# Kernel tuning notes

Hardware: AMD Instinct MI355X
Metric: run time of the kernel (lower is better)

## Reference

```python
import jax, jax.numpy as jnp
import numpy as np
from jax import lax

B, T, H, C = 64, 512, 1024, 8


def setup_inputs() -> dict:
    key = jax.random.key(0)
    ks = jax.random.split(key, 7)
    encoding = jax.random.normal(ks[0], (B, T, H), dtype=jnp.float32)
    labels = jax.random.randint(ks[1], (B, 3 * T), 0, C)
    W = jax.random.normal(ks[2], (3, C, H), dtype=jnp.float32) * 0.02
    b = jax.random.normal(ks[3], (3, C), dtype=jnp.float32) * 0.02
    start_trans = jax.random.normal(ks[4], (3, C), dtype=jnp.float32) * 0.1
    end_trans = jax.random.normal(ks[5], (3, C), dtype=jnp.float32) * 0.1
    trans = jax.random.normal(ks[6], (3, C, C), dtype=jnp.float32) * 0.1
    return {"encoding": encoding, "labels": labels, "W": W, "b": b,
            "start_trans": start_trans, "end_trans": end_trans, "trans": trans}


def crf_neg_log_lik(em, tags, start, end, trans):
    # em [B,T,C], tags [B,T] -> scalar (torchcrf reduction='sum', loss = -llh)
    bsz = em.shape[0]
    # numerator: score of gold path
    em_sc = jnp.take_along_axis(em, tags[:, :, None], axis=2)[..., 0].sum(axis=1)
    tr_sc = trans[tags[:, :-1], tags[:, 1:]].sum(axis=1)
    num = start[tags[:, 0]] + em_sc + tr_sc + end[tags[:, -1]]
    # denominator: forward algorithm (log partition)
    a0 = start[None, :] + em[:, 0]  # [B,C]

    def step(a, e_t):
        a_new = jax.nn.logsumexp(a[:, :, None] + trans[None] + e_t[:, None, :], axis=1)
        return a_new, None

    aT, _ = lax.scan(step, a0, jnp.moveaxis(em[:, 1:], 1, 0))
    logZ = jax.nn.logsumexp(aT + end[None, :], axis=1)
    return -(num - logZ).sum()


def viterbi(em, start, end, trans):
    # em [B,T,C] -> best tag path [B,T] (no mask: all sequences full length)
    v0 = start[None, :] + em[:, 0]

    def step(v, e_t):
        s = v[:, :, None] + trans[None]          # [B,C_prev,C_cur]
        bp = jnp.argmax(s, axis=1)               # [B,C]
        return jnp.max(s, axis=1) + e_t, bp

    vT, bps = lax.scan(step, v0, jnp.moveaxis(em[:, 1:], 1, 0))  # bps [T-1,B,C]
    last = jnp.argmax(vT + end[None, :], axis=1)  # [B]

    def back(tag, bp):
        prev = jnp.take_along_axis(bp, tag[:, None], axis=1)[:, 0]
        return prev, prev

    _, rev = lax.scan(back, last, bps, reverse=True)  # [T-1,B], tags for t=0..T-2
    tags = jnp.concatenate([rev, last[None]], axis=0)  # [T,B]
    return tags.T


def reference(encoding, labels, W, b, start_trans, end_trans, trans):
    # three per-task projections: logits [3,B,T,C]
    logits = jnp.einsum('bth,kch->kbtc', encoding, W) + b[:, None, None, :]
    tags = jnp.stack(jnp.split(labels, 3, axis=1))  # [3,B,T] (task/process/material)
    losses = jax.vmap(crf_neg_log_lik)(logits, tags, start_trans, end_trans, trans)
    loss = losses.sum()
    pred = jax.vmap(viterbi)(logits, start_trans, end_trans, trans)  # [3,B,T]
    return loss, logits, pred
```

## Files before the change

kernel.cpp:

```cpp
#include <hip/hip_runtime.h>

#define NB 64
#define NT 512
#define NH 1024
#define NC 8
#define NK 3
#define BT (NB*NT)
#define LOGITS_N (NK*BT*NC)

typedef unsigned short ushort;
typedef unsigned int uint;
typedef __attribute__((ext_vector_type(8))) short short8v;
typedef __attribute__((ext_vector_type(4))) float float4v;
union S8 { short8v v; ushort u[8]; };

#define QP1  0xB1
#define QP2  0x4E
#define ROR4 0x124
#define ROR8 0x128
#define HM   0x141

template<int CTRL>
__device__ __forceinline__ float dppf(float x) {
  return __int_as_float(__builtin_amdgcn_update_dpp(0, __float_as_int(x), CTRL, 0xF, 0xF, true));
}
template<int CTRL>
__device__ __forceinline__ int dppi(int x) {
  return __builtin_amdgcn_update_dpp(0, x, CTRL, 0xF, 0xF, true);
}

__device__ __forceinline__ void gload_lds16(const void* g, void* l) {
  __builtin_amdgcn_global_load_lds(
      (const __attribute__((address_space(1))) void*)g,
      (__attribute__((address_space(3))) void*)l, 16, 0, 0);
}

__global__ __launch_bounds__(256) void init_kernel(const float* __restrict__ W,
                                                   ushort* __restrict__ WB,
                                                   float* __restrict__ out) {
  const int i = blockIdx.x * 256 + threadIdx.x;
  const int ci = i >> 11;
  const int rem = i & 2047;
  const int q = rem >> 9;
  const int l = (rem >> 3) & 63;
  const int e = i & 7;
  const int k = ci * 64 + (q >> 1) * 32 + ((l >> 4) << 3) + e;
  const int j = (q & 1) * 16 + (l & 15);
  float v = 0.0f;
  if (j < 24) v = W[(j >> 3) * (NC * NH) + (j & 7) * NH + k];
  const uint b = __float_as_uint(v);
  const ushort h1 = (ushort)(b >> 16);
  const float f1 = __uint_as_float(b & 0xFFFF0000u);
  const float r1 = v - f1;
  const uint b2 = __float_as_uint(r1);
  const ushort h2 = (ushort)(b2 >> 16);
  const float f2 = __uint_as_float(b2 & 0xFFFF0000u);
  const float r2 = r1 - f2;
  const ushort h3 = (ushort)(__float_as_uint(r2) >> 16);
  WB[i] = h1;
  WB[32768 + i] = h2;
  WB[65536 + i] = h3;
  if (i == 0) out[0] = 0.0f;
}

__global__ __launch_bounds__(512, 2) void proj_kernel(const float* __restrict__ enc,
                                                      const ushort* __restrict__ WB,
                                                      const float* __restrict__ bias,
                                                      float* __restrict__ out) {
  __shared__ float  sA[2][8192];
  __shared__ ushort sB[2][6144];
  const int tid = threadIdx.x;
  const int lane = tid & 63;
  const int w = tid >> 6;
  const int row0 = blockIdx.x * 128;
  const float* eb = enc + (size_t)row0 * 1024;

  float4v acc0 = {0.0f, 0.0f, 0.0f, 0.0f};
  float4v acc1 = {0.0f, 0.0f, 0.0f, 0.0f};

  auto stageA = [&](int ci, int buf) {
#pragma unroll
    for (int i = 0; i < 4; ++i) {
      const int rbase = w * 16 + i * 4;
      const int r = rbase + (lane >> 4);
      const int s = (lane & 15) ^ (r & 15);
      gload_lds16(eb + (size_t)r * 1024 + ci * 64 + s * 4, &sA[buf][rbase * 64]);
    }
  };
  auto stageB = [&](int ci, int buf) {
    {
      const int u = w;
      gload_lds16(WB + (u >> 2) * 32768 + ci * 2048 + (u & 3) * 512 + lane * 8,
                  &sB[buf][u * 512]);
    }
    if (w < 4) {
      const int u = 8 + w;
      gload_lds16(WB + (u >> 2) * 32768 + ci * 2048 + (u & 3) * 512 + lane * 8,
                  &sB[buf][u * 512]);
    }
  };

  auto compute = [&](int buf) {
    const float* ar = &sA[buf][(w * 16 + (lane & 15)) * 64];
    const ushort* sBf = &sB[buf][0];
    const int rx = lane & 15;
    const int g = lane >> 4;
#pragma unroll
    for (int kkb = 0; kkb < 2; ++kkb) {
      const int s0 = kkb * 8 + g * 2;
      const float4 e0 = *(const float4*)&ar[(s0 ^ rx) * 4];
      const float4 e1 = *(const float4*)&ar[((s0 + 1) ^ rx) * 4];
      S8 a1, a2, a3;
      const float vals[8] = {e0.x, e0.y, e0.z, e0.w, e1.x, e1.y, e1.z, e1.w};
#pragma unroll
      for (int t = 0; t < 8; ++t) {
        const float v = vals[t];
        const uint b = __float_as_uint(v);
        a1.u[t] = (ushort)(b >> 16);
        const float f1 = __uint_as_float(b & 0xFFFF0000u);
        const float r1 = v - f1;
        const uint b2 = __float_as_uint(r1);
        a2.u[t] = (ushort)(b2 >> 16);
        const float f2 = __uint_as_float(b2 & 0xFFFF0000u);
        const float r2 = r1 - f2;
        a3.u[t] = (ushort)(__float_as_uint(r2) >> 16);
      }
#pragma unroll
      for (int jt = 0; jt < 2; ++jt) {
        const int q = kkb * 2 + jt;
        const short8v w1 = *(const short8v*)&sBf[0 * 2048 + q * 512 + lane * 8];
        const short8v w2 = *(const short8v*)&sBf[1 * 2048 + q * 512 + lane * 8];
        const short8v w3 = *(const short8v*)&sBf[2 * 2048 + q * 512 + lane * 8];
        float4v acc = jt ? acc1 : acc0;
        acc = __builtin_amdgcn_mfma_f32_16x16x32_bf16(a1.v, w1, acc, 0, 0, 0);
        acc = __builtin_amdgcn_mfma_f32_16x16x32_bf16(a2.v, w1, acc, 0, 0, 0);
        acc = __builtin_amdgcn_mfma_f32_16x16x32_bf16(a1.v, w2, acc, 0, 0, 0);
        acc = __builtin_amdgcn_mfma_f32_16x16x32_bf16(a2.v, w2, acc, 0, 0, 0);
        acc = __builtin_amdgcn_mfma_f32_16x16x32_bf16(a3.v, w1, acc, 0, 0, 0);
        acc = __builtin_amdgcn_mfma_f32_16x16x32_bf16(a1.v, w3, acc, 0, 0, 0);
        if (jt) acc1 = acc; else acc0 = acc;
      }
    }
  };

  stageA(0, 0);
  stageB(0, 0);
  __syncthreads();

#pragma unroll 1
  for (int ci = 0; ci < 16; ++ci) {
    const int buf = ci & 1;
    if (ci < 15) { stageA(ci + 1, buf ^ 1); stageB(ci + 1, buf ^ 1); }
    compute(buf);
    __syncthreads();
  }

  const int g = lane >> 4, cx = lane & 15;
#pragma unroll
  for (int jt = 0; jt < 2; ++jt) {
    const int j = jt * 16 + cx;
    if (j < 24) {
      const float bj = bias[j];
      const float4v acc = jt ? acc1 : acc0;
      float* ob = out + 1 + (size_t)(j >> 3) * (BT * 8) + (j & 7);
#pragma unroll
      for (int qq = 0; qq < 4; ++qq) {
        const int grow = row0 + w * 16 + g * 4 + qq;
        ob[(size_t)grow * 8] = acc[qq] + bj;
      }
    }
  }
}

__global__ __launch_bounds__(512) void crf_kernel(const int* __restrict__ labels,
                                                  const float* __restrict__ startT,
                                                  const float* __restrict__ endT,
                                                  const float* __restrict__ trans,
                                                  float* __restrict__ d_out) {
  __shared__ float sA[32 * 64];
  __shared__ float sVB[32 * 8];
  __shared__ int   sBP[512];
  __shared__ int   sMap[32 * 8];
  __shared__ int   sEnt[32];
  __shared__ float sRed[32];
  __shared__ unsigned char sTags[512];
  __shared__ int sTerm;

  const int tid = threadIdx.x;
  const int lane = tid & 63;
  const int w = tid >> 6;
  const int c = lane & 7;
  const int p = (lane >> 3) & 7;
  const int role = (blockIdx.x >= 192);
  const int seq = role ? blockIdx.x - 192 : blockIdx.x;
  const int k = seq >> 6, b = seq & 63;
  const float* em = d_out + 1 + ((size_t)k * BT + (size_t)b * 512) * 8;
  const float* trk = trans + k * 64;
  const int* lab = labels + b * (NK * NT) + k * NT;

  float Txc[8];
#pragma unroll
  for (int kk = 0; kk < 8; ++kk) Txc[kk] = trk[(c ^ kk) * 8 + c];
  const float Tpc = trk[p * 8 + c];
  const float startc = startT[k * 8 + c];
  const float endc = endT[k * 8 + c];

  if (!role) {
    float Mxc[8];
#pragma unroll
    for (int kk = 0; kk < 8; ++kk) Mxc[kk] = __expf(Txc[kk]);

#pragma unroll 1
    for (int it = 0; it < 4; ++it) {
      const int i = w * 4 + it;
      const int t0 = i * 16;
      const int te = (t0 + 16 < 512) ? (t0 + 16) : 511;
      float EX[16];
      EX[0] = em[(t0 + 1) * 8 + c];
#pragma unroll
      for (int j = 1; j < 16; ++j) {
        int t = t0 + 1 + j;
        EX[j] = (t <= te) ? __expf(em[t * 8 + c]) : 1.0f;
      }
      float V = __expf(Tpc + EX[0]);
#pragma unroll
      for (int j = 1; j < 16; ++j) {
        int t = t0 + 1 + j;
        if (t <= te) {
          float x1 = dppf<QP1>(V), x2 = dppf<QP2>(V), x3 = dppf<QP2>(x1);
          float x7 = dppf<HM>(V), x6 = dppf<QP1>(x7), x5 = dppf<QP2>(x7), x4 = dppf<QP2>(x6);
          float s01 = fmaf(x1, Mxc[1], V * Mxc[0]);
          float s23 = fmaf(x3, Mxc[3], x2 * Mxc[2]);
          float s45 = fmaf(x5, Mxc[5], x4 * Mxc[4]);
          float s67 = fmaf(x7, Mxc[7], x6 * Mxc[6]);
          V = ((s01 + s23) + (s45 + s67)) * EX[j];
        }
        if (j == 8) V *= 0x1p-32f;
      }
      sA[i * 64 + lane] = V;
    }
    __syncthreads();

    float logZ = 0.0f;
    if (w == 0) {
      float al = __expf(startc + em[c]);
      float lz = 0.0f;
#pragma unroll 1
      for (int i = 0; i < 32; ++i) {
        const float* Ai = &sA[i * 64];
        float A0 = Ai[(c ^ 0) * 8 + c], A1 = Ai[(c ^ 1) * 8 + c];
        float A2 = Ai[(c ^ 2) * 8 + c], A3 = Ai[(c ^ 3) * 8 + c];
        float A4 = Ai[(c ^ 4) * 8 + c], A5 = Ai[(c ^ 5) * 8 + c];
        float A6 = Ai[(c ^ 6) * 8 + c], A7 = Ai[(c ^ 7) * 8 + c];
        float a1 = dppf<QP1>(al), a2 = dppf<QP2>(al), a3 = dppf<QP2>(a1);
        float a4 = dppf<ROR4>(al), a5 = dppf<ROR4>(a1), a6 = dppf<ROR4>(a2), a7 = dppf<ROR4>(a3);
        float s01 = fmaf(a1, A1, al * A0);
        float s23 = fmaf(a3, A3, a2 * A2);
        float s45 = fmaf(a5, A5, a4 * A4);
        float s67 = fmaf(a7, A7, a6 * A6);
        float s = (s01 + s23) + (s45 + s67);
        float ss = s;
        ss += dppf<QP1>(ss); ss += dppf<QP2>(ss); ss += dppf<ROR4>(ss);
        lz += __logf(ss);
        al = s * (1.0f / ss);
      }
      float se = al * __expf(endc);
      se += dppf<QP1>(se); se += dppf<QP2>(se); se += dppf<ROR4>(se);
      logZ = lz + __logf(se) + 1024.0f * 0.69314718055994531f;
    } else {
      int idx = (w - 1) * 64 + lane;
      float ns = 0.0f;
      {
        int tg = lab[idx];
        ns += em[(size_t)idx * 8 + tg] + trk[tg * 8 + lab[idx + 1]];
      }
      if (idx < 64) {
        int t = idx + 448;
        int tg = lab[t];
        ns += em[(size_t)t * 8 + tg];
        if (t < 511) ns += trk[tg * 8 + lab[t + 1]];
      }
      ns += dppf<QP1>(ns); ns += dppf<QP2>(ns); ns += dppf<HM>(ns); ns += dppf<ROR8>(ns);
      if ((lane & 15) == 0) sRed[(w - 1) * 4 + (lane >> 4)] = ns;
    }
    __syncthreads();
    if (tid == 0) {
      float num = startT[k * 8 + lab[0]] + endT[k * 8 + lab[511]];
#pragma unroll
      for (int u = 0; u < 28; ++u) num += sRed[u];
      atomicAdd(d_out, logZ - num);
    }
  } else {
#pragma unroll 1
    for (int it = 0; it < 4; ++it) {
      const int i = w * 4 + it;
      const int t0 = i * 16;
      const int te = (t0 + 16 < 512) ? (t0 + 16) : 511;
      float emv[16];
#pragma unroll
      for (int j = 0; j < 16; ++j) {
        int t = t0 + 1 + j;
        emv[j] = (t <= te) ? em[t * 8 + c] : 0.0f;
      }
      float V = Tpc + emv[0];
#pragma unroll
      for (int j = 1; j < 16; ++j) {
        int t = t0 + 1 + j;
        if (t <= te) {
          float x1 = dppf<QP1>(V), x2 = dppf<QP2>(V), x3 = dppf<QP2>(x1);
          float x7 = dppf<HM>(V), x6 = dppf<QP1>(x7), x5 = dppf<QP2>(x7), x4 = dppf<QP2>(x6);
          float c0 = V + Txc[0], c1 = x1 + Txc[1], c2 = x2 + Txc[2], c3 = x3 + Txc[3];
          float c4 = x4 + Txc[4], c5 = x5 + Txc[5], c6 = x6 + Txc[6], c7 = x7 + Txc[7];
          float m0 = fmaxf(fmaxf(c0, c1), c2);
          float m1 = fmaxf(fmaxf(c3, c4), c5);
          float m2 = fmaxf(c6, c7);
          V = fmaxf(fmaxf(m0, m1), m2) + emv[j];
        }
      }
      sA[i * 64 + lane] = V;
    }
    __syncthreads();

    if (w == 0) {
      float v = startc + em[c];
#pragma unroll 1
      for (int i = 0; i < 32; ++i) {
        if (lane < 8) sVB[i * 8 + c] = v;
        const float* Ai = &sA[i * 64];
        float A0 = Ai[(c ^ 0) * 8 + c], A1 = Ai[(c ^ 1) * 8 + c];
        float A2 = Ai[(c ^ 2) * 8 + c], A3 = Ai[(c ^ 3) * 8 + c];
        float A4 = Ai[(c ^ 4) * 8 + c], A5 = Ai[(c ^ 5) * 8 + c];
        float A6 = Ai[(c ^ 6) * 8 + c], A7 = Ai[(c ^ 7) * 8 + c];
        float a1 = dppf<QP1>(v), a2 = dppf<QP2>(v), a3 = dppf<QP2>(a1);
        float a4 = dppf<ROR4>(v), a5 = dppf<ROR4>(a1), a6 = dppf<ROR4>(a2), a7 = dppf<ROR4>(a3);
        float c0 = v + A0, c1 = a1 + A1, c2 = a2 + A2, c3 = a3 + A3;
        float c4 = a4 + A4, c5 = a5 + A5, c6 = a6 + A6, c7 = a7 + A7;
        float m0 = fmaxf(fmaxf(c0, c1), c2);
        float m1 = fmaxf(fmaxf(c3, c4), c5);
        float m2 = fmaxf(c6, c7);
        v = fmaxf(fmaxf(m0, m1), m2);
      }
      float lv = v + endc;
      int li = c;
      {
        float ov; int oi; bool take;
        ov = dppf<QP1>(lv); oi = dppi<QP1>(li);
        take = (ov > lv) || (ov == lv && oi < li); lv = take ? ov : lv; li = take ? oi : li;
        ov = dppf<QP2>(lv); oi = dppi<QP2>(li);
        take = (ov > lv) || (ov == lv && oi < li); lv = take ? ov : lv; li = take ? oi : li;
        ov = dppf<ROR4>(lv); oi = dppi<ROR4>(li);
        take = (ov > lv) || (ov == lv && oi < li); lv = take ? ov : lv; li = take ? oi : li;
      }
      if (lane == 0) sTerm = li;
    }
    __syncthreads();

    if (w < 4) {
      const int u = lane >> 3;
      const int i = w * 8 + u;
      const int t0 = i * 16;
      const int te = (t0 + 16 < 512) ? (t0 + 16) : 511;
      float emv[16];
#pragma unroll
      for (int j = 0; j < 16; ++j) {
        int t = t0 + 1 + j;
        emv[j] = (t <= te) ? em[t * 8 + c] : 0.0f;
      }
      float v = sVB[i * 8 + c];
#pragma unroll
      for (int j = 0; j < 16; ++j) {
        int t = t0 + 1 + j;
        if (t <= te) {
          float x1 = dppf<QP1>(v), x2 = dppf<QP2>(v), x3 = dppf<QP2>(x1);
          float x7 = dppf<HM>(v), x6 = dppf<QP1>(x7), x5 = dppf<QP2>(x7), x4 = dppf<QP2>(x6);
          float c0 = v + Txc[0], c1 = x1 + Txc[1], c2 = x2 + Txc[2], c3 = x3 + Txc[3];
          float c4 = x4 + Txc[4], c5 = x5 + Txc[5], c6 = x6 + Txc[6], c7 = x7 + Txc[7];
          float m0 = fmaxf(fmaxf(c0, c1), c2);
          float m1 = fmaxf(fmaxf(c3, c4), c5);
          float m2 = fmaxf(c6, c7);
          float best = fmaxf(fmaxf(m0, m1), m2);
          int a0 = (c0 == best) ? (c ^ 0) : 8;
          int a1i = (c1 == best) ? (c ^ 1) : 8;
          int a2i = (c2 == best) ? (c ^ 2) : 8;
          int a3i = (c3 == best) ? (c ^ 3) : 8;
          int a4i = (c4 == best) ? (c ^ 4) : 8;
          int a5i = (c5 == best) ? (c ^ 5) : 8;
          int a6i = (c6 == best) ? (c ^ 6) : 8;
          int a7i = (c7 == best) ? (c ^ 7) : 8;
          int arg = min(min(min(a0, a1i), min(a2i, a3i)),
                        min(min(a4i, a5i), min(a6i, a7i)));
          v = best + emv[j];
          int wd = arg << (3 * c);
          wd |= dppi<QP1>(wd); wd |= dppi<QP2>(wd); wd |= dppi<HM>(wd);
          if ((lane & 7) == 0) sBP[t] = wd;
        }
      }
    }
    __syncthreads();

    if (w < 4) {
      const int u = lane >> 3;
      const int i = w * 8 + u;
      const int t0 = i * 16;
      const int te = (t0 + 16 < 512) ? (t0 + 16) : 511;
      int tag = c;
#pragma unroll
      for (int j = 16; j >= 1; --j) {
        int t = t0 + j;
        if (t <= te) tag = (sBP[t] >> (3 * tag)) & 7;
      }
      sMap[i * 8 + c] = tag;
    }
    __syncthreads();
    if (tid == 0) {
      int cur = sTerm;
#pragma unroll 1
      for (int i = 31; i >= 0; --i) { cur = sMap[i * 8 + cur]; sEnt[i] = cur; }
    }
    __syncthreads();
    if (w == 0 && lane < 32) {
      const int i = lane;
      const int t0 = i * 16;
      const int te = (t0 + 16 < 512) ? (t0 + 16) : 511;
      int tag = (i == 31) ? sTerm : sEnt[i + 1];
      if (i == 31) sTags[511] = (unsigned char)tag;
#pragma unroll
      for (int j = 16; j >= 1; --j) {
        int t = t0 + j;
        if (t <= te) { tag = (sBP[t] >> (3 * tag)) & 7; sTags[t - 1] = (unsigned char)tag; }
      }
    }
    __syncthreads();
    float* outp = d_out + 1 + LOGITS_N + (size_t)seq * 512;
    outp[tid] = (float)sTags[tid];
  }
}

extern "C" void kernel_launch(void* const* d_in, const int* in_sizes, int n_in,
                              void* d_out, int out_size, void* d_ws, size_t ws_size,
                              hipStream_t stream) {
  const float* enc    = (const float*)d_in[0];
  const int*   labels = (const int*)  d_in[1];
  const float* W      = (const float*)d_in[2];
  const float* bias   = (const float*)d_in[3];
  const float* startT = (const float*)d_in[4];
  const float* endT   = (const float*)d_in[5];
  const float* trans  = (const float*)d_in[6];
  float* out = (float*)d_out;
  ushort* WB = (ushort*)d_ws;

  init_kernel<<<dim3(128), dim3(256), 0, stream>>>(W, WB, out);
  proj_kernel<<<dim3(256), dim3(512), 0, stream>>>(enc, WB, bias, out);
  crf_kernel<<<dim3(384), dim3(512), 0, stream>>>(labels, startT, endT, trans, out);
}
```

Before: 238.8 us.

## Split K across waves with register-resident weights and LDS reduction

The projection kernel now gives each wave a fixed K slice of the hidden dimension. Its bf16-split weight fragments are loaded once into registers instead of being staged through LDS every chunk. Encoding rows are staged 16 at a time as full 1024-wide rows with double buffering and explicit vmcnt waits. Per-wave partial sums are reduced through LDS and written with bias, which removes the per-chunk weight LDS traffic but adds a cross-wave reduction and an extra barrier per row group, and raises register pressure.

```diff
diff --git a/kernel.cpp b/kernel.cpp
--- a/kernel.cpp
+++ b/kernel.cpp
@@ -67,107 +67,108 @@
                                                       const ushort* __restrict__ WB,
                                                       const float* __restrict__ bias,
                                                       float* __restrict__ out) {
-  __shared__ float  sA[2][8192];
-  __shared__ ushort sB[2][6144];
+  __shared__ float sA[2][16384];
+  __shared__ float sR[4096];
   const int tid = threadIdx.x;
   const int lane = tid & 63;
   const int w = tid >> 6;
   const int row0 = blockIdx.x * 128;
   const float* eb = enc + (size_t)row0 * 1024;
 
-  float4v acc0 = {0.0f, 0.0f, 0.0f, 0.0f};
-  float4v acc1 = {0.0f, 0.0f, 0.0f, 0.0f};
-
-  auto stageA = [&](int ci, int buf) {
-#pragma unroll
-    for (int i = 0; i < 4; ++i) {
-      const int rbase = w * 16 + i * 4;
-      const int r = rbase + (lane >> 4);
-      const int s = (lane & 15) ^ (r & 15);
-      gload_lds16(eb + (size_t)r * 1024 + ci * 64 + s * 4, &sA[buf][rbase * 64]);
+  short8v bf[3][4][2];
+#pragma unroll
+  for (int ks = 0; ks < 4; ++ks)
+#pragma unroll
+    for (int jt = 0; jt < 2; ++jt)
+#pragma unroll
+      for (int sp = 0; sp < 3; ++sp) {
+        const int ci = 2 * w + (ks >> 1);
+        const int q = (ks & 1) * 2 + jt;
+        bf[sp][ks][jt] = *(const short8v*)(WB + sp * 32768 + ci * 2048 + q * 512 + lane * 8);
+      }
+
+  auto stageA = [&](int rg, int buf) {
+#pragma unroll
+    for (int i = 0; i < 8; ++i) {
+      const int u = w * 8 + i;
+      const int row = u >> 2, q = u & 3;
+      gload_lds16(eb + (size_t)(rg * 16 + row) * 1024 + q * 256 + (lane ^ (row & 7)) * 4,
+                  &sA[buf][row * 1024 + q * 256]);
     }
   };
-  auto stageB = [&](int ci, int buf) {
+
+  stageA(0, 0);
+  stageA(1, 1);
+
+#pragma unroll
+  for (int rg = 0; rg < 8; ++rg) {
+    if (rg < 7) asm volatile("s_waitcnt vmcnt(8)" ::: "memory");
+    else        asm volatile("s_waitcnt vmcnt(0)" ::: "memory");
+    __builtin_amdgcn_s_barrier();
+    asm volatile("" ::: "memory");
+    __builtin_amdgcn_sched_barrier(0);
+
+    float4v a0 = {0.0f, 0.0f, 0.0f, 0.0f};
+    float4v a1c = {0.0f, 0.0f, 0.0f, 0.0f};
     {
-      const int u = w;
-      gload_lds16(WB + (u >> 2) * 32768 + ci * 2048 + (u & 3) * 512 + lane * 8,
-                  &sB[buf][u * 512]);
-    }
-    if (w < 4) {
-      const int u = 8 + w;
-      gload_lds16(WB + (u >> 2) * 32768 + ci * 2048 + (u & 3) * 512 + lane * 8,
-                  &sB[buf][u * 512]);
-    }
-  };
-
-  auto compute = [&](int buf) {
-    const float* ar = &sA[buf][(w * 16 + (lane & 15)) * 64];
-    const ushort* sBf = &sB[buf][0];
-    const int rx = lane & 15;
-    const int g = lane >> 4;
-#pragma unroll
-    for (int kkb = 0; kkb < 2; ++kkb) {
-      const int s0 = kkb * 8 + g * 2;
-      const float4 e0 = *(const float4*)&ar[(s0 ^ rx) * 4];
-      const float4 e1 = *(const float4*)&ar[((s0 + 1) ^ rx) * 4];
-      S8 a1, a2, a3;
-      const float vals[8] = {e0.x, e0.y, e0.z, e0.w, e1.x, e1.y, e1.z, e1.w};
-#pragma unroll
-      for (int t = 0; t < 8; ++t) {
-        const float v = vals[t];
-        const uint b = __float_as_uint(v);
-        a1.u[t] = (ushort)(b >> 16);
-        const float f1 = __uint_as_float(b & 0xFFFF0000u);
-        const float r1 = v - f1;
-        const uint b2 = __float_as_uint(r1);
-        a2.u[t] = (ushort)(b2 >> 16);
-        const float f2 = __uint_as_float(b2 & 0xFFFF0000u);
-        const float r2 = r1 - f2;
-        a3.u[t] = (ushort)(__float_as_uint(r2) >> 16);
-      }
-#pragma unroll
-      for (int jt = 0; jt < 2; ++jt) {
-        const int q = kkb * 2 + jt;
-        const short8v w1 = *(const short8v*)&sBf[0 * 2048 + q * 512 + lane * 8];
-        const short8v w2 = *(const short8v*)&sBf[1 * 2048 + q * 512 + lane * 8];
-        const short8v w3 = *(const short8v*)&sBf[2 * 2048 + q * 512 + lane * 8];
-        float4v acc = jt ? acc1 : acc0;
-        acc = __builtin_amdgcn_mfma_f32_16x16x32_bf16(a1.v, w1, acc, 0, 0, 0);
-        acc = __builtin_amdgcn_mfma_f32_16x16x32_bf16(a2.v, w1, acc, 0, 0, 0);
-        acc = __builtin_amdgcn_mfma_f32_16x16x32_bf16(a1.v, w2, acc, 0, 0, 0);
-        acc = __builtin_amdgcn_mfma_f32_16x16x32_bf16(a2.v, w2, acc, 0, 0, 0);
-        acc = __builtin_amdgcn_mfma_f32_16x16x32_bf16(a3.v, w1, acc, 0, 0, 0);
-        acc = __builtin_amdgcn_mfma_f32_16x16x32_bf16(a1.v, w3, acc, 0, 0, 0);
-        if (jt) acc1 = acc; else acc0 = acc;
-      }
-    }
-  };
-
-  stageA(0, 0);
-  stageB(0, 0);
-  __syncthreads();
-
-#pragma unroll 1
-  for (int ci = 0; ci < 16; ++ci) {
-    const int buf = ci & 1;
-    if (ci < 15) { stageA(ci + 1, buf ^ 1); stageB(ci + 1, buf ^ 1); }
-    compute(buf);
-    __syncthreads();
-  }
-
-  const int g = lane >> 4, cx = lane & 15;
-#pragma unroll
-  for (int jt = 0; jt < 2; ++jt) {
-    const int j = jt * 16 + cx;
-    if (j < 24) {
-      const float bj = bias[j];
-      const float4v acc = jt ? acc1 : acc0;
-      float* ob = out + 1 + (size_t)(j >> 3) * (BT * 8) + (j & 7);
-#pragma unroll
-      for (int qq = 0; qq < 4; ++qq) {
-        const int grow = row0 + w * 16 + g * 4 + qq;
-        ob[(size_t)grow * 8] = acc[qq] + bj;
-      }
+      const int r = lane & 15;
+      const int g = lane >> 4;
+      const int rx7 = r & 7;
+      const float* base = &sA[rg & 1][r * 1024];
+#pragma unroll
+      for (int ks = 0; ks < 4; ++ks) {
+        const int v = w * 32 + ks * 8 + g * 2;
+        const int q = v >> 6;
+        const int s = v & 63;
+        const float4 e0 = *(const float4*)&base[q * 256 + ((s ^ rx7) << 2)];
+        const float4 e1 = *(const float4*)&base[q * 256 + (((s + 1) ^ rx7) << 2)];
+        S8 f1a, f2a, f3a;
+        const float vals[8] = {e0.x, e0.y, e0.z, e0.w, e1.x, e1.y, e1.z, e1.w};
+#pragma unroll
+        for (int t = 0; t < 8; ++t) {
+          const float vv = vals[t];
+          const uint b = __float_as_uint(vv);
+          f1a.u[t] = (ushort)(b >> 16);
+          const float p1 = __uint_as_float(b & 0xFFFF0000u);
+          const float r1 = vv - p1;
+          const uint b2 = __float_as_uint(r1);
+          f2a.u[t] = (ushort)(b2 >> 16);
+          const float p2 = __uint_as_float(b2 & 0xFFFF0000u);
+          const float r2 = r1 - p2;
+          f3a.u[t] = (ushort)(__float_as_uint(r2) >> 16);
+        }
+#pragma unroll
+        for (int jt = 0; jt < 2; ++jt) {
+          float4v acc = jt ? a1c : a0;
+          acc = __builtin_amdgcn_mfma_f32_16x16x32_bf16(f1a.v, bf[0][ks][jt], acc, 0, 0, 0);
+          acc = __builtin_amdgcn_mfma_f32_16x16x32_bf16(f2a.v, bf[0][ks][jt], acc, 0, 0, 0);
+          acc = __builtin_amdgcn_mfma_f32_16x16x32_bf16(f1a.v, bf[1][ks][jt], acc, 0, 0, 0);
+          acc = __builtin_amdgcn_mfma_f32_16x16x32_bf16(f2a.v, bf[1][ks][jt], acc, 0, 0, 0);
+          acc = __builtin_amdgcn_mfma_f32_16x16x32_bf16(f3a.v, bf[0][ks][jt], acc, 0, 0, 0);
+          acc = __builtin_amdgcn_mfma_f32_16x16x32_bf16(f1a.v, bf[2][ks][jt], acc, 0, 0, 0);
+          if (jt) a1c = acc; else a0 = acc;
+        }
+      }
+    }
+
+    {
+      float* pw = &sR[(w * 64 + lane) * 8];
+      *(float4v*)&pw[0] = a0;
+      *(float4v*)&pw[4] = a1c;
+    }
+    asm volatile("" ::: "memory");
+    __builtin_amdgcn_s_barrier();
+    asm volatile("" ::: "memory");
+    if (rg + 2 < 8) stageA(rg + 2, rg & 1);
+
+    if (tid < 384) {
+      const int rr = tid & 15, j = tid >> 4;
+      const int lane_src = (j < 16 ? j : j - 16) + ((rr >> 2) << 4);
+      const int fi = (j < 16 ? 0 : 4) + (rr & 3);
+      float ssum = bias[j];
+#pragma unroll
+      for (int ww = 0; ww < 8; ++ww) ssum += sR[(ww * 64 + lane_src) * 8 + fi];
+      out[1 + (size_t)(j >> 3) * (BT * 8) + (size_t)(row0 + rg * 16 + rr) * 8 + (j & 7)] = ssum;
     }
   }
 }
```

Result: faster. 231.6 us (-3.0%).
